# Performance work log

Hardware: AMD Instinct MI355X
Metric: run time of the kernel (lower is better)

## Reference

```python
import jax, jax.numpy as jnp
import numpy as np

BATCH = 4096  # number of rows in the sparse input matrix (static for segment_sum)


def setup_inputs() -> dict:
    key = jax.random.key(0)
    k1, k2, k3, k4 = jax.random.split(key, 4)
    nnz = 262144
    in_features, out_features = 32000, 256
    row_idx = jnp.sort(jax.random.randint(k1, (nnz,), 0, BATCH, dtype=jnp.int32))
    col_idx = jax.random.randint(k2, (nnz,), 0, in_features, dtype=jnp.int32)
    vals = jax.random.uniform(k3, (nnz,), dtype=jnp.float32)
    weight = jax.random.normal(k4, (in_features, out_features), dtype=jnp.float32) / np.sqrt(out_features)
    bias = jnp.zeros((out_features,), dtype=jnp.float32)
    return {"row_idx": row_idx, "col_idx": col_idx, "vals": vals,
            "weight": weight, "bias": bias}


def reference(row_idx, col_idx, vals, weight, bias):
    # out = sparse_input @ weight + bias
    # sparse_input is COO: (row_idx, col_idx, vals), shape [BATCH, in_features]
    # gather weight rows for each nonzero, scale by value, sum per output row
    contrib = vals[:, None] * weight[col_idx]          # [nnz, out_features]
    out = jax.ops.segment_sum(contrib, row_idx, num_segments=BATCH)  # [BATCH, out]
    return out + bias
```

## Files before the change

kernel.cpp:

```cpp
#include <hip/hip_runtime.h>


constexpr int BATCH = 4096;

__device__ inline unsigned short f2bf(float f) {
    unsigned u = __float_as_uint(f);
    unsigned r = (u + 0x7FFFu + ((u >> 16) & 1u)) >> 16;
    return (unsigned short)r;
}

__global__ __launch_bounds__(256) void prep_kernel(
    const float* __restrict__ weight,
    unsigned short* __restrict__ wb,
    const int* __restrict__ row_idx, int nnz,
    int* __restrict__ ptr,
    int in_f, int conv_blocks)
{
    if ((int)blockIdx.x < conv_blocks) {
        const int wave = threadIdx.x >> 6;
        const int lane = threadIdx.x & 63;
        const int r    = blockIdx.x * 4 + wave;
        if (r < in_f) {
            const float4 f = reinterpret_cast<const float4*>(weight)[r * 64 + lane];
            ushort4 o;
            o.x = f2bf(f.x); o.y = f2bf(f.y); o.z = f2bf(f.z); o.w = f2bf(f.w);
            const int slice = lane >> 3;
            const size_t idx4 = ((size_t)slice * in_f + r) * 8 + (lane & 7);
            reinterpret_cast<ushort4*>(wb)[idx4] = o;
        }
    } else {
        const int i = (blockIdx.x - conv_blocks) * 256 + threadIdx.x;
        if (i >= nnz) return;
        const int r  = row_idx[i];
        const int rn = (i + 1 < nnz) ? row_idx[i + 1] : BATCH;
        for (int rr = r + 1; rr <= rn; ++rr) ptr[rr] = i + 1;
        if (i == 0)
            for (int rr = 0; rr <= r; ++rr) ptr[rr] = 0;
    }
}

__global__ __launch_bounds__(256, 8) void spmm_sliced(
    const int*            __restrict__ col_idx,
    const float*          __restrict__ vals,
    const unsigned short* __restrict__ wb,
    const float*          __restrict__ bias,
    const int*            __restrict__ ptr,
    float*                __restrict__ out,
    int nnz, int in_f)
{
    const int wave  = threadIdx.x >> 6;
    const int lane  = threadIdx.x & 63;
    const int slice = blockIdx.x & 7;
    const int r     = (blockIdx.x >> 3) * 4 + wave;

    const int start = ptr[r];
    const int end   = ptr[r + 1];

    const int j    = lane >> 4;
    const int cpos = lane & 15;

    const unsigned* __restrict__ Ws =
        reinterpret_cast<const unsigned*>(wb) + (size_t)slice * in_f * 16;

    float ax = 0.f, ay = 0.f;

    int k = start;
    for (; k + 16 <= end; k += 16) {
        #pragma unroll
        for (int t = 0; t < 4; ++t) {
            const int   kk = k + t * 4 + j;
            const int   c  = col_idx[kk];
            const float v  = vals[kk];
            const unsigned w = Ws[(size_t)c * 16 + cpos];
            ax = fmaf(v, __uint_as_float(w << 16),          ax);
            ay = fmaf(v, __uint_as_float(w & 0xFFFF0000u), ay);
        }
    }
    for (; k < end; k += 4) {
        const int   kk    = k + j;
        const bool  valid = kk < end;
        const int   c     = col_idx[valid ? kk : (nnz - 1)];
        const float v     = valid ? vals[kk] : 0.0f;
        const unsigned w  = Ws[(size_t)c * 16 + cpos];
        ax = fmaf(v, __uint_as_float(w << 16),          ax);
        ay = fmaf(v, __uint_as_float(w & 0xFFFF0000u), ay);
    }

    ax += __shfl_xor(ax, 16); ax += __shfl_xor(ax, 32);
    ay += __shfl_xor(ay, 16); ay += __shfl_xor(ay, 32);

    if (lane < 16) {
        const float2 b = reinterpret_cast<const float2*>(bias)[slice * 16 + cpos];
        float2 o; o.x = ax + b.x; o.y = ay + b.y;
        reinterpret_cast<float2*>(out)[(size_t)r * 128 + slice * 16 + cpos] = o;
    }
}

extern "C" void kernel_launch(void* const* d_in, const int* in_sizes, int n_in,
                              void* d_out, int out_size, void* d_ws, size_t ws_size,
                              hipStream_t stream)
{
    const int*   row_idx = (const int*)  d_in[0];
    const int*   col_idx = (const int*)  d_in[1];
    const float* vals    = (const float*)d_in[2];
    const float* weight  = (const float*)d_in[3];
    const float* bias    = (const float*)d_in[4];
    float*       out     = (float*)      d_out;
    const int    nnz     = in_sizes[0];
    const int    in_f    = in_sizes[3] / 256;

    unsigned short* wb      = (unsigned short*)d_ws;
    int*            row_ptr = (int*)((char*)d_ws + (32u << 20));

    const int conv_blocks = (in_f + 3) / 4;
    const int rptr_blocks = (nnz + 255) / 256;

    hipLaunchKernelGGL(prep_kernel, dim3(conv_blocks + rptr_blocks), dim3(256), 0, stream,
                       weight, wb, row_idx, nnz, row_ptr, in_f, conv_blocks);
    hipLaunchKernelGGL(spmm_sliced, dim3((BATCH / 4) * 8), dim3(256), 0, stream,
                       col_idx, vals, wb, bias, row_ptr, out, nnz, in_f);
}
```

Before: 110.0 us.

## Bind weight slices to XCCs via hardware ID and atomic work queues

The SpMM kernel now reads the XCC hardware register and uses it to pick which 8-column weight slice to process. Each XCC pulls row groups from its own atomic counter, so every XCC's L2 only holds one bf16 weight slice instead of all eight. Each lane also loads uint2 (4 bf16) rather than one packed pair, and the cross-lane reduction gains an extra shuffle stage. The design assumes exactly 8 XCCs and relies on blocks spreading evenly across them, and it adds atomic and __syncthreads overhead per row group.

```diff
diff --git a/kernel.cpp b/kernel.cpp
--- a/kernel.cpp
+++ b/kernel.cpp
@@ -2,6 +2,8 @@
 
 
 constexpr int BATCH = 4096;
+constexpr int ROWS_PER_GRP = 4;
+constexpr int NGRP = BATCH / ROWS_PER_GRP;
 
 __device__ inline unsigned short f2bf(float f) {
     unsigned u = __float_as_uint(f);
@@ -14,6 +16,7 @@
     unsigned short* __restrict__ wb,
     const int* __restrict__ row_idx, int nnz,
     int* __restrict__ ptr,
+    int* __restrict__ cnt,
     int in_f, int conv_blocks)
 {
     if ((int)blockIdx.x < conv_blocks) {
@@ -29,7 +32,9 @@
             reinterpret_cast<ushort4*>(wb)[idx4] = o;
         }
     } else {
-        const int i = (blockIdx.x - conv_blocks) * 256 + threadIdx.x;
+        const int b = (int)blockIdx.x - conv_blocks;
+        if (b == 0) cnt[threadIdx.x] = 0;
+        const int i = b * 256 + threadIdx.x;
         if (i >= nnz) return;
         const int r  = row_idx[i];
         const int rn = (i + 1 < nnz) ? row_idx[i + 1] : BATCH;
@@ -39,60 +44,85 @@
     }
 }
 
-__global__ __launch_bounds__(256, 8) void spmm_sliced(
+__device__ inline void fma4(float v, uint2 w, float4& acc) {
+    acc.x = fmaf(v, __uint_as_float(w.x << 16),          acc.x);
+    acc.y = fmaf(v, __uint_as_float(w.x & 0xFFFF0000u), acc.y);
+    acc.z = fmaf(v, __uint_as_float(w.y << 16),          acc.z);
+    acc.w = fmaf(v, __uint_as_float(w.y & 0xFFFF0000u), acc.w);
+}
+
+__global__ __launch_bounds__(256, 8) void spmm_xcc(
     const int*            __restrict__ col_idx,
     const float*          __restrict__ vals,
     const unsigned short* __restrict__ wb,
     const float*          __restrict__ bias,
     const int*            __restrict__ ptr,
+    int*                  __restrict__ cnt,
     float*                __restrict__ out,
-    int nnz, int in_f)
+    int in_f)
 {
-    const int wave  = threadIdx.x >> 6;
-    const int lane  = threadIdx.x & 63;
-    const int slice = blockIdx.x & 7;
-    const int r     = (blockIdx.x >> 3) * 4 + wave;
+    __shared__ int s_grp;
 
-    const int start = ptr[r];
-    const int end   = ptr[r + 1];
+    const int wave = threadIdx.x >> 6;
+    const int lane = threadIdx.x & 63;
+    const int j    = lane >> 3;
+    const int cpos = lane & 7;
 
-    const int j    = lane >> 4;
-    const int cpos = lane & 15;
+    unsigned xcc;
+    asm volatile("s_getreg_b32 %0, hwreg(HW_REG_XCC_ID)" : "=s"(xcc));
+    const int slice = (int)(xcc & 7u);
 
-    const unsigned* __restrict__ Ws =
-        reinterpret_cast<const unsigned*>(wb) + (size_t)slice * in_f * 16;
+    const uint2* __restrict__ Ws =
+        reinterpret_cast<const uint2*>(wb) + (size_t)slice * in_f * 8;
+    const float4 b = reinterpret_cast<const float4*>(bias)[slice * 8 + cpos];
 
-    float ax = 0.f, ay = 0.f;
+    for (;;) {
+        __syncthreads();
+        if (threadIdx.x == 0)
+            s_grp = atomicAdd(&cnt[slice * 32], 1);
+        __syncthreads();
+        const int grp = s_grp;
+        if (grp >= NGRP) break;
 
-    int k = start;
-    for (; k + 16 <= end; k += 16) {
-        #pragma unroll
-        for (int t = 0; t < 4; ++t) {
-            const int   kk = k + t * 4 + j;
-            const int   c  = col_idx[kk];
-            const float v  = vals[kk];
-            const unsigned w = Ws[(size_t)c * 16 + cpos];
-            ax = fmaf(v, __uint_as_float(w << 16),          ax);
-            ay = fmaf(v, __uint_as_float(w & 0xFFFF0000u), ay);
+        const int r     = grp * ROWS_PER_GRP + wave;
+        const int start = ptr[r];
+        const int end   = ptr[r + 1];
+
+        float4 acc = make_float4(0.f, 0.f, 0.f, 0.f);
+
+        int k = start;
+        for (; k + 16 <= end; k += 16) {
+            const int   c0 = col_idx[k + j];
+            const float v0 = vals[k + j];
+            const int   c1 = col_idx[k + 8 + j];
+            const float v1 = vals[k + 8 + j];
+            const uint2 w0 = Ws[(size_t)c0 * 8 + cpos];
+            const uint2 w1 = Ws[(size_t)c1 * 8 + cpos];
+            fma4(v0, w0, acc);
+            fma4(v1, w1, acc);
         }
-    }
-    for (; k < end; k += 4) {
-        const int   kk    = k + j;
-        const bool  valid = kk < end;
-        const int   c     = col_idx[valid ? kk : (nnz - 1)];
-        const float v     = valid ? vals[kk] : 0.0f;
-        const unsigned w  = Ws[(size_t)c * 16 + cpos];
-        ax = fmaf(v, __uint_as_float(w << 16),          ax);
-        ay = fmaf(v, __uint_as_float(w & 0xFFFF0000u), ay);
-    }
+        for (; k < end; k += 8) {
+            const int  kk    = k + j;
+            const bool valid = kk < end;
+            const int   c = col_idx[valid ? kk : start];
+            const float v = valid ? vals[kk] : 0.0f;
+            const uint2 w = Ws[(size_t)c * 8 + cpos];
+            fma4(v, w, acc);
+        }
 
-    ax += __shfl_xor(ax, 16); ax += __shfl_xor(ax, 32);
-    ay += __shfl_xor(ay, 16); ay += __shfl_xor(ay, 32);
+        acc.x += __shfl_xor(acc.x, 8);  acc.y += __shfl_xor(acc.y, 8);
+        acc.z += __shfl_xor(acc.z, 8);  acc.w += __shfl_xor(acc.w, 8);
+        acc.x += __shfl_xor(acc.x, 16); acc.y += __shfl_xor(acc.y, 16);
+        acc.z += __shfl_xor(acc.z, 16); acc.w += __shfl_xor(acc.w, 16);
+        acc.x += __shfl_xor(acc.x, 32); acc.y += __shfl_xor(acc.y, 32);
+        acc.z += __shfl_xor(acc.z, 32); acc.w += __shfl_xor(acc.w, 32);
 
-    if (lane < 16) {
-        const float2 b = reinterpret_cast<const float2*>(bias)[slice * 16 + cpos];
-        float2 o; o.x = ax + b.x; o.y = ay + b.y;
-        reinterpret_cast<float2*>(out)[(size_t)r * 128 + slice * 16 + cpos] = o;
+        if (lane < 8) {
+            float4 o;
+            o.x = acc.x + b.x; o.y = acc.y + b.y;
+            o.z = acc.z + b.z; o.w = acc.w + b.w;
+            reinterpret_cast<float4*>(out)[(size_t)r * 64 + slice * 8 + lane] = o;
+        }
     }
 }
 
@@ -111,12 +141,13 @@
 
     unsigned short* wb      = (unsigned short*)d_ws;
     int*            row_ptr = (int*)((char*)d_ws + (32u << 20));
+    int*            cnt     = (int*)((char*)d_ws + (48u << 20));
 
     const int conv_blocks = (in_f + 3) / 4;
     const int rptr_blocks = (nnz + 255) / 256;
 
     hipLaunchKernelGGL(prep_kernel, dim3(conv_blocks + rptr_blocks), dim3(256), 0, stream,
-                       weight, wb, row_idx, nnz, row_ptr, in_f, conv_blocks);
-    hipLaunchKernelGGL(spmm_sliced, dim3((BATCH / 4) * 8), dim3(256), 0, stream,
-                       col_idx, vals, wb, bias, row_ptr, out, nnz, in_f);
+                       weight, wb, row_idx, nnz, row_ptr, cnt, in_f, conv_blocks);
+    hipLaunchKernelGGL(spmm_xcc, dim3(2048), dim3(256), 0, stream,
+                       col_idx, vals, wb, bias, row_ptr, cnt, out, in_f);
 }
```

Result: slower. 119.5 us (+8.6%).

## Quantize weight to per-row int8 and restructure SpMM with split-row waves

Applied to the files above, without the earlier changes.

Replaces the bf16 weight copy with per-row symmetric int8 quantization plus a per-row scale, which halves the bytes gathered per nonzero. The scale is folded into the values in a separate prep kernel. The SpMM kernel is restructured so each lane handles 8 output columns and two waves split each row's nonzeros, with the partial sums combined through shared memory. This adds a third kernel launch, and int8 loses much more precision than bf16, which risks exceeding the accuracy tolerance.

```diff
diff --git a/kernel.cpp b/kernel.cpp
--- a/kernel.cpp
+++ b/kernel.cpp
@@ -3,17 +3,12 @@
 
 constexpr int BATCH = 4096;
 
-__device__ inline unsigned short f2bf(float f) {
-    unsigned u = __float_as_uint(f);
-    unsigned r = (u + 0x7FFFu + ((u >> 16) & 1u)) >> 16;
-    return (unsigned short)r;
-}
-
-__global__ __launch_bounds__(256) void prep_kernel(
+__global__ __launch_bounds__(256) void prep_quant(
     const float* __restrict__ weight,
-    unsigned short* __restrict__ wb,
-    const int* __restrict__ row_idx, int nnz,
-    int* __restrict__ ptr,
+    unsigned*    __restrict__ wq,
+    float*       __restrict__ scale,
+    const int*   __restrict__ row_idx, int nnz,
+    int*         __restrict__ ptr,
     int in_f, int conv_blocks)
 {
     if ((int)blockIdx.x < conv_blocks) {
@@ -22,14 +17,24 @@
         const int r    = blockIdx.x * 4 + wave;
         if (r < in_f) {
             const float4 f = reinterpret_cast<const float4*>(weight)[r * 64 + lane];
-            ushort4 o;
-            o.x = f2bf(f.x); o.y = f2bf(f.y); o.z = f2bf(f.z); o.w = f2bf(f.w);
-            const int slice = lane >> 3;
-            const size_t idx4 = ((size_t)slice * in_f + r) * 8 + (lane & 7);
-            reinterpret_cast<ushort4*>(wb)[idx4] = o;
+            float m = fmaxf(fmaxf(fabsf(f.x), fabsf(f.y)),
+                            fmaxf(fabsf(f.z), fabsf(f.w)));
+            #pragma unroll
+            for (int o = 32; o; o >>= 1) m = fmaxf(m, __shfl_xor(m, o));
+            const float inv = (m > 0.f) ? 127.0f / m : 0.0f;
+            const int q0 = (int)rintf(f.x * inv);
+            const int q1 = (int)rintf(f.y * inv);
+            const int q2 = (int)rintf(f.z * inv);
+            const int q3 = (int)rintf(f.w * inv);
+            const unsigned p = ( (unsigned)q0        & 0xFFu)
+                             | (((unsigned)q1 & 0xFFu) <<  8)
+                             | (((unsigned)q2 & 0xFFu) << 16)
+                             | (((unsigned)q3 & 0xFFu) << 24);
+            wq[(size_t)r * 64 + lane] = p;
+            if (lane == 0) scale[r] = (m > 0.f) ? m / 127.0f : 0.0f;
         }
     } else {
-        const int i = (blockIdx.x - conv_blocks) * 256 + threadIdx.x;
+        const int i = ((int)blockIdx.x - conv_blocks) * 256 + threadIdx.x;
         if (i >= nnz) return;
         const int r  = row_idx[i];
         const int rn = (i + 1 < nnz) ? row_idx[i + 1] : BATCH;
@@ -39,60 +44,103 @@
     }
 }
 
-__global__ __launch_bounds__(256, 8) void spmm_sliced(
-    const int*            __restrict__ col_idx,
-    const float*          __restrict__ vals,
-    const unsigned short* __restrict__ wb,
-    const float*          __restrict__ bias,
-    const int*            __restrict__ ptr,
-    float*                __restrict__ out,
-    int nnz, int in_f)
+__global__ __launch_bounds__(256) void prep_vals(
+    const int*   __restrict__ col_idx,
+    const float* __restrict__ vals,
+    const float* __restrict__ scale,
+    float*       __restrict__ vsc, int nnz)
 {
-    const int wave  = threadIdx.x >> 6;
-    const int lane  = threadIdx.x & 63;
-    const int slice = blockIdx.x & 7;
-    const int r     = (blockIdx.x >> 3) * 4 + wave;
+    const int i = blockIdx.x * 256 + threadIdx.x;
+    if (i < nnz) vsc[i] = vals[i] * scale[col_idx[i]];
+}
+
+__device__ inline void fma8(float v, uint2 w, float* acc) {
+    const unsigned ux = w.x, uy = w.y;
+    acc[0] = fmaf(v, (float)((int)(ux << 24) >> 24), acc[0]);
+    acc[1] = fmaf(v, (float)((int)(ux << 16) >> 24), acc[1]);
+    acc[2] = fmaf(v, (float)((int)(ux <<  8) >> 24), acc[2]);
+    acc[3] = fmaf(v, (float)((int) ux        >> 24), acc[3]);
+    acc[4] = fmaf(v, (float)((int)(uy << 24) >> 24), acc[4]);
+    acc[5] = fmaf(v, (float)((int)(uy << 16) >> 24), acc[5]);
+    acc[6] = fmaf(v, (float)((int)(uy <<  8) >> 24), acc[6]);
+    acc[7] = fmaf(v, (float)((int) uy        >> 24), acc[7]);
+}
+
+__global__ __launch_bounds__(256, 8) void spmm_i8(
+    const int*      __restrict__ col_idx,
+    const float*    __restrict__ vsc,
+    const unsigned* __restrict__ wq,
+    const float*    __restrict__ bias,
+    const int*      __restrict__ ptr,
+    float*          __restrict__ out)
+{
+    __shared__ float part[4][32][8];
+
+    const int wave = threadIdx.x >> 6;
+    const int lane = threadIdx.x & 63;
+    const int r    = blockIdx.x * 2 + (wave >> 1);
+    const int half = wave & 1;
+    const int h32  = lane >> 5;
+    const int c32  = lane & 31;
 
     const int start = ptr[r];
     const int end   = ptr[r + 1];
+    const int chunk = (end - start + 1) >> 1;
 
-    const int j    = lane >> 4;
-    const int cpos = lane & 15;
+    int k  = start + half * chunk;
+    const int ke = min(k + chunk, end);
 
-    const unsigned* __restrict__ Ws =
-        reinterpret_cast<const unsigned*>(wb) + (size_t)slice * in_f * 16;
+    const uint2* __restrict__ W2 = reinterpret_cast<const uint2*>(wq);
 
-    float ax = 0.f, ay = 0.f;
+    float acc[8] = {0.f, 0.f, 0.f, 0.f, 0.f, 0.f, 0.f, 0.f};
 
-    int k = start;
-    for (; k + 16 <= end; k += 16) {
+    while (k + 16 <= ke) {
+        int cs[8]; float vs[8]; uint2 ws[8];
         #pragma unroll
-        for (int t = 0; t < 4; ++t) {
-            const int   kk = k + t * 4 + j;
-            const int   c  = col_idx[kk];
-            const float v  = vals[kk];
-            const unsigned w = Ws[(size_t)c * 16 + cpos];
-            ax = fmaf(v, __uint_as_float(w << 16),          ax);
-            ay = fmaf(v, __uint_as_float(w & 0xFFFF0000u), ay);
+        for (int t = 0; t < 8; ++t) {
+            const int kk = k + 2 * t + h32;
+            cs[t] = col_idx[kk];
+            vs[t] = vsc[kk];
         }
+        #pragma unroll
+        for (int t = 0; t < 8; ++t)
+            ws[t] = W2[(size_t)cs[t] * 32 + c32];
+        #pragma unroll
+        for (int t = 0; t < 8; ++t)
+            fma8(vs[t], ws[t], acc);
+        k += 16;
     }
-    for (; k < end; k += 4) {
-        const int   kk    = k + j;
-        const bool  valid = kk < end;
-        const int   c     = col_idx[valid ? kk : (nnz - 1)];
-        const float v     = valid ? vals[kk] : 0.0f;
-        const unsigned w  = Ws[(size_t)c * 16 + cpos];
-        ax = fmaf(v, __uint_as_float(w << 16),          ax);
-        ay = fmaf(v, __uint_as_float(w & 0xFFFF0000u), ay);
+    while (k < ke) {
+        const int  kk    = k + h32;
+        const bool valid = kk < ke;
+        const int   c = col_idx[valid ? kk : start];
+        const float v = valid ? vsc[kk] : 0.0f;
+        const uint2 w = W2[(size_t)c * 32 + c32];
+        fma8(v, w, acc);
+        k += 2;
     }
 
-    ax += __shfl_xor(ax, 16); ax += __shfl_xor(ax, 32);
-    ay += __shfl_xor(ay, 16); ay += __shfl_xor(ay, 32);
+    #pragma unroll
+    for (int d = 0; d < 8; ++d) acc[d] += __shfl_xor(acc[d], 32);
 
-    if (lane < 16) {
-        const float2 b = reinterpret_cast<const float2*>(bias)[slice * 16 + cpos];
-        float2 o; o.x = ax + b.x; o.y = ay + b.y;
-        reinterpret_cast<float2*>(out)[(size_t)r * 128 + slice * 16 + cpos] = o;
+    if (lane < 32) {
+        #pragma unroll
+        for (int d = 0; d < 8; ++d) part[wave][lane][d] = acc[d];
+    }
+    __syncthreads();
+
+    if (threadIdx.x < 128) {
+        const int rl = threadIdx.x >> 6;
+        const int ln = threadIdx.x & 63;
+        const int ci = ln >> 1;
+        const int co = (ln & 1) * 4;
+        const float4 b = reinterpret_cast<const float4*>(bias)[ln];
+        float4 o;
+        o.x = part[2*rl][ci][co+0] + part[2*rl+1][ci][co+0] + b.x;
+        o.y = part[2*rl][ci][co+1] + part[2*rl+1][ci][co+1] + b.y;
+        o.z = part[2*rl][ci][co+2] + part[2*rl+1][ci][co+2] + b.z;
+        o.w = part[2*rl][ci][co+3] + part[2*rl+1][ci][co+3] + b.w;
+        reinterpret_cast<float4*>(out)[(size_t)(blockIdx.x * 2 + rl) * 64 + ln] = o;
     }
 }
 
@@ -109,14 +157,18 @@
     const int    nnz     = in_sizes[0];
     const int    in_f    = in_sizes[3] / 256;
 
-    unsigned short* wb      = (unsigned short*)d_ws;
-    int*            row_ptr = (int*)((char*)d_ws + (32u << 20));
+    unsigned* wq      = (unsigned*)d_ws;
+    float*    scale   = (float*)((char*)d_ws + (12u << 20));
+    int*      row_ptr = (int*)  ((char*)d_ws + (13u << 20));
+    float*    vsc     = (float*)((char*)d_ws + (14u << 20));
 
     const int conv_blocks = (in_f + 3) / 4;
     const int rptr_blocks = (nnz + 255) / 256;
 
-    hipLaunchKernelGGL(prep_kernel, dim3(conv_blocks + rptr_blocks), dim3(256), 0, stream,
-                       weight, wb, row_idx, nnz, row_ptr, in_f, conv_blocks);
-    hipLaunchKernelGGL(spmm_sliced, dim3((BATCH / 4) * 8), dim3(256), 0, stream,
-                       col_idx, vals, wb, bias, row_ptr, out, nnz, in_f);
+    hipLaunchKernelGGL(prep_quant, dim3(conv_blocks + rptr_blocks), dim3(256), 0, stream,
+                       weight, wq, scale, row_idx, nnz, row_ptr, in_f, conv_blocks);
+    hipLaunchKernelGGL(prep_vals, dim3((nnz + 255) / 256), dim3(256), 0, stream,
+                       col_idx, vals, scale, vsc, nnz);
+    hipLaunchKernelGGL(spmm_i8, dim3(BATCH / 2), dim3(256), 0, stream,
+                       col_idx, vsc, wq, bias, row_ptr, out);
 }
```

New measurement: 104.0 us. -5.4%, faster.
